# Kernel tuning notes

Measured on AMD Instinct MI355X. Metric: run time of the kernel, lower is better.

The kernel has to match this reference:

```python
import jax, jax.numpy as jnp
import numpy as np

N_NODES = 100000
N_EDGES = 640000
D_IN = 128
D_OUT = 128
EPS = 1e-5


def setup_inputs() -> dict:
    key = jax.random.key(0)
    k_h, k_src, k_dst, k_ws, k_wn = jax.random.split(key, 5)
    h = jax.random.normal(k_h, (N_NODES, D_IN), dtype=jnp.float32)
    src = jax.random.randint(k_src, (N_EDGES,), 0, N_NODES, dtype=jnp.int32)
    dst = jax.random.randint(k_dst, (N_EDGES,), 0, N_NODES, dtype=jnp.int32)
    gamma = jnp.ones((D_IN,), dtype=jnp.float32)
    beta = jnp.zeros((D_IN,), dtype=jnp.float32)
    scale = 1.0 / np.sqrt(D_IN)
    W_self = jax.random.normal(k_ws, (D_IN, D_OUT), dtype=jnp.float32) * scale
    W_neigh = jax.random.normal(k_wn, (D_IN, D_OUT), dtype=jnp.float32) * scale
    b = jnp.zeros((D_OUT,), dtype=jnp.float32)
    return {"h": h, "src": src, "dst": dst, "gamma": gamma, "beta": beta,
            "W_self": W_self, "W_neigh": W_neigh, "b": b}


def reference(h, src, dst, gamma, beta, W_self, W_neigh, b):
    # LayerNorm over feature dim
    mu = jnp.mean(h, axis=-1, keepdims=True)
    var = jnp.mean(jnp.square(h - mu), axis=-1, keepdims=True)
    hn = (h - mu) * jax.lax.rsqrt(var + EPS) * gamma + beta  # [N, D_IN]

    n = h.shape[0]
    # mean-aggregate messages from src -> dst (zero for isolated nodes, DGL semantics)
    msg_sum = jax.ops.segment_sum(hn[src], dst, num_segments=n)     # [N, D_IN]
    deg = jax.ops.segment_sum(jnp.ones_like(dst, dtype=hn.dtype), dst, num_segments=n)
    h_neigh = msg_sum / jnp.maximum(deg, 1.0)[:, None]

    # SAGEConv: fc_self(h) + fc_neigh(h_neigh) + bias; dropout is identity at eval/p=0
    out = hn @ W_self + h_neigh @ W_neigh + b
    return out
```

## Files before the change

### kernel.cpp

```cpp
#include <hip/hip_runtime.h>
#include <hip/hip_bf16.h>

#define D 128
#define CAP 64

typedef __attribute__((ext_vector_type(8))) short bf16x8;
typedef __attribute__((ext_vector_type(4))) float f32x4;
typedef __attribute__((ext_vector_type(4))) int i32x4;

__device__ __forceinline__ float bf2f(ushort u) { return __uint_as_float(((unsigned)u) << 16); }
__device__ __forceinline__ ushort f2bf(float f) {
  unsigned x = __float_as_uint(f);
  x += 0x7fffu + ((x >> 16) & 1u);
  return (ushort)(x >> 16);
}

__device__ __forceinline__ bool detect_bf16(const unsigned* __restrict__ h) {
  unsigned w = h[threadIdx.x & 63];
  unsigned e = (w >> 7) & 0xFFu;
  unsigned long long m = __ballot(e >= 0x60u && e <= 0x8Fu);
  return __popcll(m) >= 32;
}

__global__ __launch_bounds__(256) void combo_kernel(
    const int* __restrict__ src, const int* __restrict__ dst,
    int* __restrict__ cnt, int* __restrict__ slots, int nE, int nbB, int nbW,
    const void* __restrict__ hv, const void* __restrict__ gv,
    const void* __restrict__ bv, ushort* __restrict__ hn, int n,
    const void* __restrict__ Wselfv, const void* __restrict__ Wneighv,
    ushort* __restrict__ WF)
{
  int b = blockIdx.x, t = threadIdx.x;
  if (b < nbB) {
    int ds[4], ss[4];
#pragma unroll
    for (int i = 0; i < 4; ++i) {
      int e = b * 1024 + i * 256 + t;
      ds[i] = (e < nE) ? dst[e] : -1;
      ss[i] = (e < nE) ? src[e] : 0;
    }
    int ps[4];
#pragma unroll
    for (int i = 0; i < 4; ++i)
      ps[i] = (ds[i] >= 0) ? atomicAdd(&cnt[ds[i]], 1) : CAP;
#pragma unroll
    for (int i = 0; i < 4; ++i)
      if (ds[i] >= 0 && ps[i] < CAP) slots[(size_t)ds[i] * CAP + ps[i]] = ss[i];
    return;
  }
  if (b < nbB + nbW) {
    bool isbf = detect_bf16((const unsigned*)hv);
    int i = (b - nbB) * 256 + t;
    int b2 = i & 7;
    int ln = (i >> 3) & 63;
    int nt = (i >> 9) & 7;
    int ks = i >> 12;
    int col = nt * 16 + (ln & 15);
    int k = ks * 32 + ((ln >> 4) << 3) + b2;
    size_t idx = (k < D) ? ((size_t)k * D + col) : ((size_t)(k - D) * D + col);
    const void* W = (k < D) ? Wselfv : Wneighv;
    ushort w;
    if (isbf) w = ((const ushort*)W)[idx];
    else      w = f2bf(((const float*)W)[idx]);
    WF[i] = w;
    return;
  }
  bool isbf = detect_bf16((const unsigned*)hv);
  int base = (b - nbB - nbW) * 64;
  int wave = t >> 6, lane = t & 63;
#pragma unroll
  for (int it = 0; it < 4; ++it) {
    if (isbf) {
      int row = base + it * 16 + wave * 4 + (lane >> 4);
      int fo = (lane & 15) * 8;
      if (row < n) {
        bf16x8 u = *(const bf16x8*)((const ushort*)hv + (size_t)row * D + fo);
        float x[8], s = 0.f, sq = 0.f;
#pragma unroll
        for (int i = 0; i < 8; ++i) { x[i] = bf2f((ushort)u[i]); s += x[i]; sq += x[i] * x[i]; }
#pragma unroll
        for (int m = 1; m < 16; m <<= 1) { s += __shfl_xor(s, m); sq += __shfl_xor(sq, m); }
        float mu  = s * (1.0f / D);
        float var = sq * (1.0f / D) - mu * mu;
        float inv = rsqrtf(var + 1e-5f);
        bf16x8 g = *(const bf16x8*)((const ushort*)gv + fo);
        bf16x8 be = *(const bf16x8*)((const ushort*)bv + fo);
        bf16x8 o;
#pragma unroll
        for (int i = 0; i < 8; ++i)
          o[i] = (short)f2bf((x[i] - mu) * inv * bf2f((ushort)g[i]) + bf2f((ushort)be[i]));
        *(bf16x8*)(hn + (size_t)row * D + fo) = o;
      }
    } else {
#pragma unroll
      for (int sub = 0; sub < 2; ++sub) {
        int row = base + it * 16 + wave * 4 + sub * 2 + (lane >> 5);
        int fo = (lane & 31) * 4;
        if (row < n) {
          float4 u = *(const float4*)((const float*)hv + (size_t)row * D + fo);
          float s  = (u.x + u.y) + (u.z + u.w);
          float sq = (u.x * u.x + u.y * u.y) + (u.z * u.z + u.w * u.w);
#pragma unroll
          for (int m = 1; m < 32; m <<= 1) { s += __shfl_xor(s, m); sq += __shfl_xor(sq, m); }
          float mu  = s * (1.0f / D);
          float var = sq * (1.0f / D) - mu * mu;
          float inv = rsqrtf(var + 1e-5f);
          float4 g = *(const float4*)((const float*)gv + fo);
          float4 be = *(const float4*)((const float*)bv + fo);
          ushort4 o;
          o.x = f2bf((u.x - mu) * inv * g.x + be.x);
          o.y = f2bf((u.y - mu) * inv * g.y + be.y);
          o.z = f2bf((u.z - mu) * inv * g.z + be.z);
          o.w = f2bf((u.w - mu) * inv * g.w + be.w);
          *(ushort4*)(hn + (size_t)row * D + fo) = o;
        }
      }
    }
  }
}

__global__ __launch_bounds__(256) void aggregate_kernel(
    const ushort* __restrict__ hn, const int* __restrict__ cnt,
    int* __restrict__ padhm, int n)
{
  int node = blockIdx.x * 4 + (threadIdx.x >> 6);
  int lane = threadIdx.x & 63;
  if (node >= n) return;
  int fl = lane & 15;
  int g  = lane >> 4;
  int dg = cnt[node];
  int dgc = dg < CAP ? dg : CAP;
  const int* slots = padhm + (size_t)node * CAP;
  float a[8];
#pragma unroll
  for (int i = 0; i < 8; ++i) a[i] = 0.f;

  int j = g;
  for (; j + 4 < dgc; j += 8) {
    int s0 = slots[j], s1 = slots[j + 4];
    bf16x8 u0 = *(const bf16x8*)(hn + (size_t)s0 * D + fl * 8);
    bf16x8 u1 = *(const bf16x8*)(hn + (size_t)s1 * D + fl * 8);
#pragma unroll
    for (int i = 0; i < 8; ++i) a[i] += bf2f((ushort)u0[i]) + bf2f((ushort)u1[i]);
  }
  if (j < dgc) {
    int s0 = slots[j];
    bf16x8 u0 = *(const bf16x8*)(hn + (size_t)s0 * D + fl * 8);
#pragma unroll
    for (int i = 0; i < 8; ++i) a[i] += bf2f((ushort)u0[i]);
  }
#pragma unroll
  for (int i = 0; i < 8; ++i) {
    a[i] += __shfl_xor(a[i], 16);
    a[i] += __shfl_xor(a[i], 32);
  }
  if (g == 0) {
    float invd = 1.0f / (float)(dg > 1 ? dg : 1);
    bf16x8 o;
#pragma unroll
    for (int i = 0; i < 8; ++i) o[i] = (short)f2bf(a[i] * invd);
    *(bf16x8*)((ushort*)padhm + (size_t)node * D + fl * 8) = o;
  }
}

__global__ __launch_bounds__(256) void gemm_kernel(
    const ushort* __restrict__ hn, const ushort* __restrict__ hm,
    const ushort* __restrict__ WF, const void* __restrict__ biasv,
    const void* __restrict__ hv, void* __restrict__ outv, int n)
{
  __shared__ __align__(16) char LDSb[32768];
  bool isbf = detect_bf16((const unsigned*)hv);
  int t = threadIdx.x;
  int wave = t >> 6, lane = t & 63;
  int R0 = blockIdx.x * 64;

  bf16x8 bfr[8][2];
#pragma unroll
  for (int ks = 0; ks < 8; ++ks)
#pragma unroll
    for (int q = 0; q < 2; ++q)
      bfr[ks][q] = ((const bf16x8*)WF)[(ks * 8 + wave * 2 + q) * 64 + lane];

  int o0 = t * 16,            o1 = 4096 + t * 16;
  int row0 = o0 >> 7,         row1 = o1 >> 7;
  int off0 = o0 & 127,        off1 = o1 & 127;
  int l0 = row0 * 128 + (off0 ^ ((row0 & 7) << 4));
  int l1 = row1 * 128 + (off1 ^ ((row1 & 7) << 4));
  int gr0 = R0 + row0,        gr1 = R0 + row1;

  uint4 s0, s1;
  auto stage_load = [&](int c, uint4& v0, uint4& v1) {
    const ushort* srcb = (c < 2) ? hn : hm;
    int cb = (c & 1) * 128;
    uint4 z; z.x = z.y = z.z = z.w = 0u;
    v0 = (gr0 < n) ? *(const uint4*)((const char*)(srcb + (size_t)gr0 * D) + cb + off0) : z;
    v1 = (gr1 < n) ? *(const uint4*)((const char*)(srcb + (size_t)gr1 * D) + cb + off1) : z;
  };

  int rl = lane & 15;
  int kb = (lane >> 4) << 4;

  f32x4 acc[4][2];
#pragma unroll
  for (int m = 0; m < 4; ++m)
#pragma unroll
    for (int q = 0; q < 2; ++q) acc[m][q] = (f32x4)0.0f;

  stage_load(0, s0, s1);
  *(uint4*)(LDSb + l0) = s0;
  *(uint4*)(LDSb + l1) = s1;
  __syncthreads();

  for (int c = 0; c < 4; ++c) {
    uint4 n0, n1;
    if (c < 3) stage_load(c + 1, n0, n1);
    int bufo = (c & 1) * 8192;
#pragma unroll
    for (int kl = 0; kl < 2; ++kl) {
      bf16x8 a[4];
#pragma unroll
      for (int m = 0; m < 4; ++m) {
        int row = m * 16 + rl;
        int off = kl * 64 + kb;
        a[m] = *(const bf16x8*)(LDSb + bufo + row * 128 + (off ^ ((row & 7) << 4)));
      }
      int ks = c * 2 + kl;
#pragma unroll
      for (int q = 0; q < 2; ++q)
#pragma unroll
        for (int m = 0; m < 4; ++m)
          acc[m][q] = __builtin_amdgcn_mfma_f32_16x16x32_bf16(a[m], bfr[ks][q], acc[m][q], 0, 0, 0);
    }
    if (c < 3) {
      int nb2 = ((c + 1) & 1) * 8192;
      *(uint4*)(LDSb + nb2 + l0) = n0;
      *(uint4*)(LDSb + nb2 + l1) = n1;
      __syncthreads();
    }
  }
  __syncthreads();

  int ocol = lane & 15;
  float bi0, bi1;
  {
    int co0 = wave * 32 + ocol, co1 = co0 + 16;
    if (isbf) { bi0 = bf2f(((const ushort*)biasv)[co0]); bi1 = bf2f(((const ushort*)biasv)[co1]); }
    else      { bi0 = ((const float*)biasv)[co0];        bi1 = ((const float*)biasv)[co1]; }
  }
  if (isbf) {
    ushort* E = (ushort*)(LDSb + wave * 8192);
#pragma unroll
    for (int q = 0; q < 2; ++q) {
      float bi = q ? bi1 : bi0;
#pragma unroll
      for (int m = 0; m < 4; ++m)
#pragma unroll
        for (int b2 = 0; b2 < 4; ++b2) {
          int row = m * 16 + ((lane >> 4) << 2) + b2;
          E[row * 32 + q * 16 + ocol] = f2bf(acc[m][q][b2] + bi);
        }
    }
    __builtin_amdgcn_s_barrier();
#pragma unroll
    for (int i = 0; i < 4; ++i) {
      int flat = i * 64 + lane;
      int row  = flat >> 2;
      int cb2  = (flat & 3) * 8;
      int ro = R0 + row;
      if (ro < n) {
        i32x4 v = *(const i32x4*)(&E[row * 32 + cb2]);
        __builtin_nontemporal_store(v, (i32x4*)((ushort*)outv + (size_t)ro * D + wave * 32 + cb2));
      }
    }
  } else {
    float* E = (float*)(LDSb + wave * 8192);
#pragma unroll
    for (int q = 0; q < 2; ++q) {
      float bi = q ? bi1 : bi0;
#pragma unroll
      for (int m = 0; m < 4; ++m)
#pragma unroll
        for (int b2 = 0; b2 < 4; ++b2) {
          int row = m * 16 + ((lane >> 4) << 2) + b2;
          E[row * 32 + q * 16 + ocol] = acc[m][q][b2] + bi;
        }
    }
    __builtin_amdgcn_s_barrier();
#pragma unroll
    for (int i = 0; i < 8; ++i) {
      int flat = i * 64 + lane;
      int row  = flat >> 3;
      int ch   = (flat & 7) * 4;
      int ro = R0 + row;
      if (ro < n) {
        f32x4 v = *(const f32x4*)(&E[row * 32 + ch]);
        __builtin_nontemporal_store(v, (f32x4*)((float*)outv + (size_t)ro * D + wave * 32 + ch));
      }
    }
  }
}

extern "C" void kernel_launch(void* const* d_in, const int* in_sizes, int n_in,
                              void* d_out, int out_size, void* d_ws, size_t ws_size,
                              hipStream_t stream) {
  const void* h      = d_in[0];
  const int*  src    = (const int*)d_in[1];
  const int*  dst    = (const int*)d_in[2];
  const void* gamma  = d_in[3];
  const void* beta   = d_in[4];
  const void* Wself  = d_in[5];
  const void* Wneigh = d_in[6];
  const void* bias   = d_in[7];

  int nNodes = in_sizes[0] / D;
  int nEdges = in_sizes[1];

  char* ws = (char*)d_ws;
  size_t p = 0;
  auto alloc = [&](size_t bytes) { char* r = ws + p; p = (p + bytes + 255) & ~(size_t)255; return r; };
  ushort* hn    = (ushort*)alloc((size_t)nNodes * D * sizeof(ushort));
  int*   padhm  = (int*)alloc((size_t)nNodes * CAP * sizeof(int));
  int*   cnt    = (int*)alloc((size_t)nNodes * sizeof(int));
  ushort* WF    = (ushort*)alloc(32768 * sizeof(ushort));

  hipMemsetAsync(cnt, 0, (size_t)nNodes * sizeof(int), stream);

  int nbB = (nEdges + 1023) / 1024;
  int nbW = 128;
  int nbL = (nNodes + 63) / 64;
  combo_kernel<<<nbB + nbW + nbL, 256, 0, stream>>>(
      src, dst, cnt, padhm, nEdges, nbB, nbW,
      h, gamma, beta, hn, nNodes, Wself, Wneigh, WF);

  aggregate_kernel<<<(nNodes + 3) / 4, 256, 0, stream>>>(hn, cnt, padhm, nNodes);

  gemm_kernel<<<(nNodes + 63) / 64, 256, 0, stream>>>(hn, (const ushort*)padhm, WF,
                                                      bias, h, d_out, nNodes);
}
```

Measured before the change: 110.0 us.

## Fold LayerNorm into GEMM epilogue and gather raw rows with per-node stats

Drops the materialized normalized feature buffer. Per-row mean and inverse-std are computed into a small stats array, and gamma is folded into W_self, with a correction vector u and a fused bias (beta·W_self + b). The self GEMM then runs on raw h and applies inv*(acc - mu*u) + bias2 in the epilogue. Aggregation gathers raw h rows and normalizes each neighbour with its stats, applying gamma and beta once after the mean. This removes a full N×D bf16 write and read, but in fp32 mode the gathers read fp32 rows, doubling the bytes read per gathered row.

New measurement: 135.5 us. 23.2% more time.

```diff
diff --git a/kernel.cpp b/kernel.cpp
--- a/kernel.cpp
+++ b/kernel.cpp
@@ -24,13 +24,82 @@
 
 __global__ __launch_bounds__(256) void combo_kernel(
     const int* __restrict__ src, const int* __restrict__ dst,
-    int* __restrict__ cnt, int* __restrict__ slots, int nE, int nbB, int nbW,
+    int* __restrict__ cnt, int* __restrict__ slots, int nE, int nbS, int nbB, int nbW,
     const void* __restrict__ hv, const void* __restrict__ gv,
-    const void* __restrict__ bv, ushort* __restrict__ hn, int n,
+    const void* __restrict__ bv, const void* __restrict__ biasv,
+    float2* __restrict__ stats, int n,
     const void* __restrict__ Wselfv, const void* __restrict__ Wneighv,
-    ushort* __restrict__ WF)
+    ushort* __restrict__ WF, float* __restrict__ u, float* __restrict__ bias2)
 {
   int b = blockIdx.x, t = threadIdx.x;
+  if (b < nbS) {
+    bool isbf = detect_bf16((const unsigned*)hv);
+    int base = b * 64;
+    int wave = t >> 6, lane = t & 63;
+    int grp = lane >> 4, fl = lane & 15;
+    if (isbf) {
+      int fo = fl * 8;
+      int r0 = base + wave * 16 + grp * 4;
+      const ushort* hp = (const ushort*)hv;
+      bf16x8 v[4];
+#pragma unroll
+      for (int i = 0; i < 4; ++i)
+        v[i] = (r0 + i < n) ? *(const bf16x8*)(hp + (size_t)(r0 + i) * D + fo) : (bf16x8)0;
+      float s[4], sq[4];
+#pragma unroll
+      for (int i = 0; i < 4; ++i) {
+        s[i] = 0.f; sq[i] = 0.f;
+#pragma unroll
+        for (int k = 0; k < 8; ++k) {
+          float x = bf2f((ushort)v[i][k]);
+          s[i] += x; sq[i] += x * x;
+        }
+      }
+#pragma unroll
+      for (int m = 1; m < 16; m <<= 1)
+#pragma unroll
+        for (int i = 0; i < 4; ++i) {
+          s[i] += __shfl_xor(s[i], m); sq[i] += __shfl_xor(sq[i], m);
+        }
+      if (fl == 0) {
+#pragma unroll
+        for (int i = 0; i < 4; ++i) {
+          if (r0 + i < n) {
+            float mu = s[i] * (1.0f / D);
+            float inv = rsqrtf(sq[i] * (1.0f / D) - mu * mu + 1e-5f);
+            stats[r0 + i] = make_float2(mu, inv);
+          }
+        }
+      }
+    } else {
+      const float* hp = (const float*)hv;
+      int el = fl * 8;
+#pragma unroll
+      for (int it = 0; it < 2; ++it) {
+        int rA = base + wave * 16 + it * 8 + grp * 2;
+#pragma unroll
+        for (int rr = 0; rr < 2; ++rr) {
+          int r = rA + rr;
+          if (r < n) {
+            float4 a0 = *(const float4*)(hp + (size_t)r * D + el);
+            float4 a1 = *(const float4*)(hp + (size_t)r * D + el + 4);
+            float s  = (a0.x + a0.y + a0.z + a0.w) + (a1.x + a1.y + a1.z + a1.w);
+            float sq = (a0.x*a0.x + a0.y*a0.y + a0.z*a0.z + a0.w*a0.w)
+                     + (a1.x*a1.x + a1.y*a1.y + a1.z*a1.z + a1.w*a1.w);
+#pragma unroll
+            for (int m = 1; m < 16; m <<= 1) { s += __shfl_xor(s, m); sq += __shfl_xor(sq, m); }
+            if (fl == 0) {
+              float mu = s * (1.0f / D);
+              float inv = rsqrtf(sq * (1.0f / D) - mu * mu + 1e-5f);
+              stats[r] = make_float2(mu, inv);
+            }
+          }
+        }
+      }
+    }
+    return;
+  }
+  b -= nbS;
   if (b < nbB) {
     int ds[4], ss[4];
 #pragma unroll
@@ -48,86 +117,60 @@
       if (ds[i] >= 0 && ps[i] < CAP) slots[(size_t)ds[i] * CAP + ps[i]] = ss[i];
     return;
   }
-  if (b < nbB + nbW) {
+  b -= nbB;
+  if (b < nbW) {
     bool isbf = detect_bf16((const unsigned*)hv);
-    int i = (b - nbB) * 256 + t;
+    int i = b * 256 + t;
     int b2 = i & 7;
     int ln = (i >> 3) & 63;
     int nt = (i >> 9) & 7;
     int ks = i >> 12;
     int col = nt * 16 + (ln & 15);
     int k = ks * 32 + ((ln >> 4) << 3) + b2;
-    size_t idx = (k < D) ? ((size_t)k * D + col) : ((size_t)(k - D) * D + col);
-    const void* W = (k < D) ? Wselfv : Wneighv;
-    ushort w;
-    if (isbf) w = ((const ushort*)W)[idx];
-    else      w = f2bf(((const float*)W)[idx]);
-    WF[i] = w;
+    bool self = (k < D);
+    size_t idx = self ? ((size_t)k * D + col) : ((size_t)(k - D) * D + col);
+    const void* W = self ? Wselfv : Wneighv;
+    float wv = isbf ? bf2f(((const ushort*)W)[idx]) : ((const float*)W)[idx];
+    if (self) {
+      float gk = isbf ? bf2f(((const ushort*)gv)[k]) : ((const float*)gv)[k];
+      wv *= gk;
+    }
+    WF[i] = f2bf(wv);
     return;
   }
-  bool isbf = detect_bf16((const unsigned*)hv);
-  int base = (b - nbB - nbW) * 64;
-  int wave = t >> 6, lane = t & 63;
-#pragma unroll
-  for (int it = 0; it < 4; ++it) {
-    if (isbf) {
-      int row = base + it * 16 + wave * 4 + (lane >> 4);
-      int fo = (lane & 15) * 8;
-      if (row < n) {
-        bf16x8 u = *(const bf16x8*)((const ushort*)hv + (size_t)row * D + fo);
-        float x[8], s = 0.f, sq = 0.f;
-#pragma unroll
-        for (int i = 0; i < 8; ++i) { x[i] = bf2f((ushort)u[i]); s += x[i]; sq += x[i] * x[i]; }
-#pragma unroll
-        for (int m = 1; m < 16; m <<= 1) { s += __shfl_xor(s, m); sq += __shfl_xor(sq, m); }
-        float mu  = s * (1.0f / D);
-        float var = sq * (1.0f / D) - mu * mu;
-        float inv = rsqrtf(var + 1e-5f);
-        bf16x8 g = *(const bf16x8*)((const ushort*)gv + fo);
-        bf16x8 be = *(const bf16x8*)((const ushort*)bv + fo);
-        bf16x8 o;
-#pragma unroll
-        for (int i = 0; i < 8; ++i)
-          o[i] = (short)f2bf((x[i] - mu) * inv * bf2f((ushort)g[i]) + bf2f((ushort)be[i]));
-        *(bf16x8*)(hn + (size_t)row * D + fo) = o;
-      }
-    } else {
-#pragma unroll
-      for (int sub = 0; sub < 2; ++sub) {
-        int row = base + it * 16 + wave * 4 + sub * 2 + (lane >> 5);
-        int fo = (lane & 31) * 4;
-        if (row < n) {
-          float4 u = *(const float4*)((const float*)hv + (size_t)row * D + fo);
-          float s  = (u.x + u.y) + (u.z + u.w);
-          float sq = (u.x * u.x + u.y * u.y) + (u.z * u.z + u.w * u.w);
-#pragma unroll
-          for (int m = 1; m < 32; m <<= 1) { s += __shfl_xor(s, m); sq += __shfl_xor(sq, m); }
-          float mu  = s * (1.0f / D);
-          float var = sq * (1.0f / D) - mu * mu;
-          float inv = rsqrtf(var + 1e-5f);
-          float4 g = *(const float4*)((const float*)gv + fo);
-          float4 be = *(const float4*)((const float*)bv + fo);
-          ushort4 o;
-          o.x = f2bf((u.x - mu) * inv * g.x + be.x);
-          o.y = f2bf((u.y - mu) * inv * g.y + be.y);
-          o.z = f2bf((u.z - mu) * inv * g.z + be.z);
-          o.w = f2bf((u.w - mu) * inv * g.w + be.w);
-          *(ushort4*)(hn + (size_t)row * D + fo) = o;
-        }
-      }
+  {
+    bool isbf = detect_bf16((const unsigned*)hv);
+    int c = t & 127;
+    bool doU = t < 128;
+    float acc = 0.f;
+#pragma unroll 4
+    for (int k = 0; k < D; ++k) {
+      float w = isbf ? bf2f(((const ushort*)Wselfv)[(size_t)k * D + c])
+                     : ((const float*)Wselfv)[(size_t)k * D + c];
+      float coef;
+      if (doU) coef = isbf ? bf2f(((const ushort*)gv)[k]) : ((const float*)gv)[k];
+      else     coef = isbf ? bf2f(((const ushort*)bv)[k]) : ((const float*)bv)[k];
+      acc += coef * w;
+    }
+    if (doU) u[c] = acc;
+    else {
+      float bc = isbf ? bf2f(((const ushort*)biasv)[c]) : ((const float*)biasv)[c];
+      bias2[c] = acc + bc;
     }
   }
 }
 
 __global__ __launch_bounds__(256) void aggregate_kernel(
-    const ushort* __restrict__ hn, const int* __restrict__ cnt,
-    int* __restrict__ padhm, int n)
+    const void* __restrict__ hv, const float2* __restrict__ stats,
+    const void* __restrict__ gv, const void* __restrict__ bv,
+    const int* __restrict__ cnt, int* __restrict__ padhm, int n)
 {
   int node = blockIdx.x * 4 + (threadIdx.x >> 6);
   int lane = threadIdx.x & 63;
   if (node >= n) return;
+  bool isbf = detect_bf16((const unsigned*)hv);
   int fl = lane & 15;
-  int g  = lane >> 4;
+  int g4 = lane >> 4;
   int dg = cnt[node];
   int dgc = dg < CAP ? dg : CAP;
   const int* slots = padhm + (size_t)node * CAP;
@@ -135,38 +178,72 @@
 #pragma unroll
   for (int i = 0; i < 8; ++i) a[i] = 0.f;
 
-  int j = g;
-  for (; j + 4 < dgc; j += 8) {
-    int s0 = slots[j], s1 = slots[j + 4];
-    bf16x8 u0 = *(const bf16x8*)(hn + (size_t)s0 * D + fl * 8);
-    bf16x8 u1 = *(const bf16x8*)(hn + (size_t)s1 * D + fl * 8);
-#pragma unroll
-    for (int i = 0; i < 8; ++i) a[i] += bf2f((ushort)u0[i]) + bf2f((ushort)u1[i]);
-  }
-  if (j < dgc) {
-    int s0 = slots[j];
-    bf16x8 u0 = *(const bf16x8*)(hn + (size_t)s0 * D + fl * 8);
-#pragma unroll
-    for (int i = 0; i < 8; ++i) a[i] += bf2f((ushort)u0[i]);
+  if (isbf) {
+    const ushort* hp = (const ushort*)hv;
+    int j = g4;
+    for (; j + 4 < dgc; j += 8) {
+      int s0 = slots[j], s1 = slots[j + 4];
+      float2 st0 = stats[s0], st1 = stats[s1];
+      bf16x8 u0 = *(const bf16x8*)(hp + (size_t)s0 * D + fl * 8);
+      bf16x8 u1 = *(const bf16x8*)(hp + (size_t)s1 * D + fl * 8);
+#pragma unroll
+      for (int i = 0; i < 8; ++i)
+        a[i] += (bf2f((ushort)u0[i]) - st0.x) * st0.y + (bf2f((ushort)u1[i]) - st1.x) * st1.y;
+    }
+    if (j < dgc) {
+      int s0 = slots[j];
+      float2 st0 = stats[s0];
+      bf16x8 u0 = *(const bf16x8*)(hp + (size_t)s0 * D + fl * 8);
+#pragma unroll
+      for (int i = 0; i < 8; ++i) a[i] += (bf2f((ushort)u0[i]) - st0.x) * st0.y;
+    }
+  } else {
+    const float* hp = (const float*)hv;
+    for (int j = g4; j < dgc; j += 4) {
+      int s0 = slots[j];
+      float2 st0 = stats[s0];
+      float4 v0 = *(const float4*)(hp + (size_t)s0 * D + fl * 8);
+      float4 v1 = *(const float4*)(hp + (size_t)s0 * D + fl * 8 + 4);
+      a[0] += (v0.x - st0.x) * st0.y; a[1] += (v0.y - st0.x) * st0.y;
+      a[2] += (v0.z - st0.x) * st0.y; a[3] += (v0.w - st0.x) * st0.y;
+      a[4] += (v1.x - st0.x) * st0.y; a[5] += (v1.y - st0.x) * st0.y;
+      a[6] += (v1.z - st0.x) * st0.y; a[7] += (v1.w - st0.x) * st0.y;
+    }
   }
 #pragma unroll
   for (int i = 0; i < 8; ++i) {
     a[i] += __shfl_xor(a[i], 16);
     a[i] += __shfl_xor(a[i], 32);
   }
-  if (g == 0) {
+  if (g4 == 0) {
     float invd = 1.0f / (float)(dg > 1 ? dg : 1);
+    float gf[8], bef[8];
+    if (isbf) {
+      bf16x8 g8 = *(const bf16x8*)((const ushort*)gv + fl * 8);
+      bf16x8 b8 = *(const bf16x8*)((const ushort*)bv + fl * 8);
+#pragma unroll
+      for (int i = 0; i < 8; ++i) { gf[i] = bf2f((ushort)g8[i]); bef[i] = bf2f((ushort)b8[i]); }
+    } else {
+      float4 g0 = *(const float4*)((const float*)gv + fl * 8);
+      float4 g1 = *(const float4*)((const float*)gv + fl * 8 + 4);
+      float4 b0 = *(const float4*)((const float*)bv + fl * 8);
+      float4 b1 = *(const float4*)((const float*)bv + fl * 8 + 4);
+      gf[0]=g0.x; gf[1]=g0.y; gf[2]=g0.z; gf[3]=g0.w; gf[4]=g1.x; gf[5]=g1.y; gf[6]=g1.z; gf[7]=g1.w;
+      bef[0]=b0.x; bef[1]=b0.y; bef[2]=b0.z; bef[3]=b0.w; bef[4]=b1.x; bef[5]=b1.y; bef[6]=b1.z; bef[7]=b1.w;
+    }
     bf16x8 o;
 #pragma unroll
-    for (int i = 0; i < 8; ++i) o[i] = (short)f2bf(a[i] * invd);
+    for (int i = 0; i < 8; ++i)
+      o[i] = (short)((dg > 0) ? f2bf(gf[i] * (a[i] * invd) + bef[i]) : (ushort)0);
     *(bf16x8*)((ushort*)padhm + (size_t)node * D + fl * 8) = o;
   }
 }
 
 __global__ __launch_bounds__(256) void gemm_kernel(
-    const ushort* __restrict__ hn, const ushort* __restrict__ hm,
-    const ushort* __restrict__ WF, const void* __restrict__ biasv,
-    const void* __restrict__ hv, void* __restrict__ outv, int n)
+    const void* __restrict__ hv, const ushort* __restrict__ hm,
+    const float2* __restrict__ stats, const ushort* __restrict__ WF,
+    const float* __restrict__ u, const float* __restrict__ bias2,
+    void* __restrict__ outv, int n)
 {
   __shared__ __align__(16) char LDSb[32768];
   bool isbf = detect_bf16((const unsigned*)hv);
@@ -188,17 +265,40 @@
   int l1 = row1 * 128 + (off1 ^ ((row1 & 7) << 4));
   int gr0 = R0 + row0,        gr1 = R0 + row1;
 
+  auto pack_f32 = [&](const float* p) {
+    float4 a = *(const float4*)p;
+    float4 c = *(const float4*)(p + 4);
+    uint4 r;
+    r.x = (unsigned)f2bf(a.x) | ((unsigned)f2bf(a.y) << 16);
+    r.y = (unsigned)f2bf(a.z) | ((unsigned)f2bf(a.w) << 16);
+    r.z = (unsigned)f2bf(c.x) | ((unsigned)f2bf(c.y) << 16);
+    r.w = (unsigned)f2bf(c.z) | ((unsigned)f2bf(c.w) << 16);
+    return r;
+  };
   uint4 s0, s1;
   auto stage_load = [&](int c, uint4& v0, uint4& v1) {
-    const ushort* srcb = (c < 2) ? hn : hm;
     int cb = (c & 1) * 128;
     uint4 z; z.x = z.y = z.z = z.w = 0u;
-    v0 = (gr0 < n) ? *(const uint4*)((const char*)(srcb + (size_t)gr0 * D) + cb + off0) : z;
-    v1 = (gr1 < n) ? *(const uint4*)((const char*)(srcb + (size_t)gr1 * D) + cb + off1) : z;
+    if (c < 2) {
+      if (isbf) {
+        const ushort* hp = (const ushort*)hv;
+        v0 = (gr0 < n) ? *(const uint4*)((const char*)(hp + (size_t)gr0 * D) + cb + off0) : z;
+        v1 = (gr1 < n) ? *(const uint4*)((const char*)(hp + (size_t)gr1 * D) + cb + off1) : z;
+      } else {
+        const float* hp = (const float*)hv;
+        v0 = (gr0 < n) ? pack_f32(hp + (size_t)gr0 * D + ((cb + off0) >> 1)) : z;
+        v1 = (gr1 < n) ? pack_f32(hp + (size_t)gr1 * D + ((cb + off1) >> 1)) : z;
+      }
+    } else {
+      v0 = (gr0 < n) ? *(const uint4*)((const char*)(hm + (size_t)gr0 * D) + cb + off0) : z;
+      v1 = (gr1 < n) ? *(const uint4*)((const char*)(hm + (size_t)gr1 * D) + cb + off1) : z;
+    }
   };
 
   int rl = lane & 15;
   int kb = (lane >> 4) << 4;
+  int ocol = lane & 15;
+  int orow4 = (lane >> 4) << 2;
 
   f32x4 acc[4][2];
 #pragma unroll
@@ -230,6 +330,24 @@
 #pragma unroll
         for (int m = 0; m < 4; ++m)
           acc[m][q] = __builtin_amdgcn_mfma_f32_16x16x32_bf16(a[m], bfr[ks][q], acc[m][q], 0, 0, 0);
+    }
+    if (c == 1) {
+      float uu[2], bb[2];
+#pragma unroll
+      for (int q = 0; q < 2; ++q) {
+        int co = wave * 32 + q * 16 + ocol;
+        uu[q] = u[co]; bb[q] = bias2[co];
+      }
+#pragma unroll
+      for (int m = 0; m < 4; ++m)
+#pragma unroll
+        for (int b2 = 0; b2 < 4; ++b2) {
+          int r = R0 + m * 16 + orow4 + b2;
+          float2 st = (r < n) ? stats[r] : make_float2(0.f, 1.f);
+#pragma unroll
+          for (int q = 0; q < 2; ++q)
+            acc[m][q][b2] = st.y * (acc[m][q][b2] - st.x * uu[q]) + bb[q];
+        }
     }
     if (c < 3) {
       int nb2 = ((c + 1) & 1) * 8192;
@@ -240,26 +358,17 @@
   }
   __syncthreads();
 
-  int ocol = lane & 15;
-  float bi0, bi1;
-  {
-    int co0 = wave * 32 + ocol, co1 = co0 + 16;
-    if (isbf) { bi0 = bf2f(((const ushort*)biasv)[co0]); bi1 = bf2f(((const ushort*)biasv)[co1]); }
-    else      { bi0 = ((const float*)biasv)[co0];        bi1 = ((const float*)biasv)[co1]; }
-  }
   if (isbf) {
     ushort* E = (ushort*)(LDSb + wave * 8192);
 #pragma unroll
-    for (int q = 0; q < 2; ++q) {
-      float bi = q ? bi1 : bi0;
+    for (int q = 0; q < 2; ++q)
 #pragma unroll
       for (int m = 0; m < 4; ++m)
 #pragma unroll
         for (int b2 = 0; b2 < 4; ++b2) {
-          int row = m * 16 + ((lane >> 4) << 2) + b2;
-          E[row * 32 + q * 16 + ocol] = f2bf(acc[m][q][b2] + bi);
-        }
-    }
+          int row = m * 16 + orow4 + b2;
+          E[row * 32 + q * 16 + ocol] = f2bf(acc[m][q][b2]);
+        }
     __builtin_amdgcn_s_barrier();
 #pragma unroll
     for (int i = 0; i < 4; ++i) {
@@ -275,16 +384,14 @@
   } else {
     float* E = (float*)(LDSb + wave * 8192);
 #pragma unroll
-    for (int q = 0; q < 2; ++q) {
-      float bi = q ? bi1 : bi0;
+    for (int q = 0; q < 2; ++q)
 #pragma unroll
       for (int m = 0; m < 4; ++m)
 #pragma unroll
         for (int b2 = 0; b2 < 4; ++b2) {
-          int row = m * 16 + ((lane >> 4) << 2) + b2;
-          E[row * 32 + q * 16 + ocol] = acc[m][q][b2] + bi;
-        }
-    }
+          int row = m * 16 + orow4 + b2;
+          E[row * 32 + q * 16 + ocol] = acc[m][q][b2];
+        }
     __builtin_amdgcn_s_barrier();
 #pragma unroll
     for (int i = 0; i < 8; ++i) {
@@ -318,22 +425,25 @@
   char* ws = (char*)d_ws;
   size_t p = 0;
   auto alloc = [&](size_t bytes) { char* r = ws + p; p = (p + bytes + 255) & ~(size_t)255; return r; };
-  ushort* hn    = (ushort*)alloc((size_t)nNodes * D * sizeof(ushort));
-  int*   padhm  = (int*)alloc((size_t)nNodes * CAP * sizeof(int));
-  int*   cnt    = (int*)alloc((size_t)nNodes * sizeof(int));
+  int*    padhm = (int*)alloc((size_t)nNodes * CAP * sizeof(int));
+  int*    cnt   = (int*)alloc((size_t)nNodes * sizeof(int));
+  float2* stats = (float2*)alloc((size_t)nNodes * sizeof(float2));
   ushort* WF    = (ushort*)alloc(32768 * sizeof(ushort));
+  float*  u     = (float*)alloc(128 * sizeof(float));
+  float*  bias2 = (float*)alloc(128 * sizeof(float));
 
   hipMemsetAsync(cnt, 0, (size_t)nNodes * sizeof(int), stream);
 
+  int nbS = (nNodes + 63) / 64;
   int nbB = (nEdges + 1023) / 1024;
   int nbW = 128;
-  int nbL = (nNodes + 63) / 64;
-  combo_kernel<<<nbB + nbW + nbL, 256, 0, stream>>>(
-      src, dst, cnt, padhm, nEdges, nbB, nbW,
-      h, gamma, beta, hn, nNodes, Wself, Wneigh, WF);
-
-  aggregate_kernel<<<(nNodes + 3) / 4, 256, 0, stream>>>(hn, cnt, padhm, nNodes);
-
-  gemm_kernel<<<(nNodes + 63) / 64, 256, 0, stream>>>(hn, (const ushort*)padhm, WF,
-                                                      bias, h, d_out, nNodes);
-}
+  combo_kernel<<<nbS + nbB + nbW + 1, 256, 0, stream>>>(
+      src, dst, cnt, padhm, nEdges, nbS, nbB, nbW,
+      h, gamma, beta, bias, stats, nNodes, Wself, Wneigh, WF, u, bias2);
+
+  aggregate_kernel<<<(nNodes + 3) / 4, 256, 0, stream>>>(h, stats, gamma, beta,
+                                                         cnt, padhm, nNodes);
+
+  gemm_kernel<<<(nNodes + 63) / 64, 256, 0, stream>>>(h, (const ushort*)padhm, stats,
+                                                      WF, u, bias2, d_out, nNodes);
+}
```
